# Kernel tuning notes

Hardware: AMD Instinct MI355X
Metric: run time of the kernel (lower is better)

Reference implementation:

```python
import jax, jax.numpy as jnp
import numpy as np

B, S, D, H = 2, 2048, 768, 12
DK = D // H
NEG = -10000.0


def setup_inputs() -> dict:
    key = jax.random.key(0)
    ks = jax.random.split(key, 12)
    def lin(k):
        kw, kb = jax.random.split(k)
        return (jax.random.normal(kw, (D, D), jnp.float32) * 0.02,
                jax.random.normal(kb, (D,), jnp.float32) * 0.02)
    Wq, bq = lin(ks[0]); Wk, bk = lin(ks[1]); Wv, bv = lin(ks[2]); Wo, bo = lin(ks[3])
    query = jax.random.normal(ks[4], (B, S, D), jnp.float32)
    key_t = jax.random.normal(ks[5], (B, S, D), jnp.float32)
    value = jax.random.normal(ks[6], (B, S, D), jnp.float32)
    # causal mask, broadcastable to [B,H,S,S]; positions with 0 are masked
    mask = jnp.tril(jnp.ones((S, S), jnp.int32))[None, None, :, :]
    return {"query": query, "key": key_t, "value": value, "mask": mask,
            "Wq": Wq, "bq": bq, "Wk": Wk, "bk": bk, "Wv": Wv, "bv": bv,
            "Wo": Wo, "bo": bo}


def reference(query, key, value, mask, Wq, bq, Wk, bk, Wv, bv, Wo, bo):
    # torch.nn.Linear: y = x @ W^T + b
    def split_heads(x):  # [B,S,D] -> [B,H,S,DK]
        return x.reshape(B, S, H, DK).transpose(0, 2, 1, 3)
    q = split_heads(query @ Wq.T + bq)
    k = split_heads(key @ Wk.T + bk)
    v = split_heads(value @ Wv.T + bv)
    scores = jnp.einsum('bhqd,bhkd->bhqk', q, k) / jnp.sqrt(jnp.float32(DK))
    scores = jnp.where(mask == 0, NEG, scores)  # masked_fill(mask==0, -1e4)
    attn = jax.nn.softmax(scores, axis=-1)      # dropout p=0.0 -> identity
    x = jnp.einsum('bhqk,bhkd->bhqd', attn, v)  # [B,H,S,DK]
    x = x.transpose(0, 2, 1, 3).reshape(B, S, D)
    return x @ Wo.T + bo
```

## Files before the change

kernel.cpp:

```cpp
#include <hip/hip_runtime.h>
#include <cstdint>


#define B_ 2
#define S_ 2048
#define D_ 768
#define H_ 12
#define DK_ 64

typedef __bf16 bf16;
typedef __bf16 bf16x8 __attribute__((ext_vector_type(8)));
typedef float f32x4 __attribute__((ext_vector_type(4)));
typedef uint32_t u32x4 __attribute__((ext_vector_type(4)));

__device__ __forceinline__ f32x4 mfma16(bf16x8 a, bf16x8 b, f32x4 c) {
  return __builtin_amdgcn_mfma_f32_16x16x32_bf16(a, b, c, 0, 0, 0);
}

struct raw8 { u32x4 a, b; };

__device__ __forceinline__ raw8 fetch8(const void* base, size_t off, int isbf) {
  raw8 r;
  if (isbf) {
    r.a = *(const u32x4*)((const bf16*)base + off);
  } else {
    const float* f = (const float*)base + off;
    r.a = *(const u32x4*)f;
    r.b = *(const u32x4*)(f + 4);
  }
  return r;
}

__device__ __forceinline__ bf16x8 cvt8(raw8 r, int isbf) {
  if (isbf) return __builtin_bit_cast(bf16x8, r.a);
  const float4 x = __builtin_bit_cast(float4, r.a);
  const float4 y = __builtin_bit_cast(float4, r.b);
  bf16x8 o;
  o[0]=(bf16)x.x; o[1]=(bf16)x.y; o[2]=(bf16)x.z; o[3]=(bf16)x.w;
  o[4]=(bf16)y.x; o[5]=(bf16)y.y; o[6]=(bf16)y.z; o[7]=(bf16)y.w;
  return o;
}

__device__ __forceinline__ float load_scalar(const void* base, int idx, int isbf) {
  return isbf ? (float)((const bf16*)base)[idx] : ((const float*)base)[idx];
}

__global__ void detect_kernel(const uint32_t* __restrict__ q, int* flag) {
  __shared__ int cnt;
  if (threadIdx.x == 0) cnt = 0;
  __syncthreads();
  int local = 0;
  for (int i = (int)threadIdx.x; i < 1024; i += 256) {
    const uint32_t e = (q[i] >> 7) & 0xff;
    if (e >= 96 && e <= 140) local++;
  }
  atomicAdd(&cnt, local);
  __syncthreads();
  if (threadIdx.x == 0) *flag = (cnt >= 600) ? 1 : 0;
}

__global__ __launch_bounds__(256) void qkv_kernel(
    const void* __restrict__ q, const void* __restrict__ k,
    const void* __restrict__ v,
    const void* __restrict__ Wq, const void* __restrict__ Wk,
    const void* __restrict__ Wv,
    const void* __restrict__ bq, const void* __restrict__ bk,
    const void* __restrict__ bv,
    bf16* __restrict__ qh, bf16* __restrict__ kh, bf16* __restrict__ vt,
    const int* __restrict__ flag)
{
  __shared__ __align__(16) bf16 As[128][40];
  __shared__ __align__(16) bf16 Bs[64][40];
  const int isbf = *flag;
  const int z = (int)blockIdx.z;
  const void* X = (z == 0) ? q : (z == 1) ? k : v;
  const void* W = (z == 0) ? Wq : (z == 1) ? Wk : Wv;
  const void* bias = (z == 0) ? bq : (z == 1) ? bk : bv;
  bf16* out = (z == 0) ? qh : (z == 1) ? kh : vt;
  const int mode = (z == 2) ? 1 : 0;

  const int m0 = blockIdx.x * 128;
  const int h = (int)blockIdx.y;
  const int n0 = h * 64;
  const int t = (int)threadIdx.x;
  const int lane = t & 63, w = t >> 6, c = lane & 15, quad = lane >> 4;
  const int ar = t >> 2, as = (t & 3) * 8;

  f32x4 acc[2][4];
#pragma unroll
  for (int mt = 0; mt < 2; ++mt)
#pragma unroll
    for (int nb = 0; nb < 4; ++nb)
#pragma unroll
      for (int i = 0; i < 4; ++i) acc[mt][nb][i] = 0.0f;

  raw8 pa0 = fetch8(X, (size_t)(m0 + ar) * D_ + as, isbf);
  raw8 pa1 = fetch8(X, (size_t)(m0 + 64 + ar) * D_ + as, isbf);
  raw8 pb  = fetch8(W, (size_t)(n0 + ar) * D_ + as, isbf);

  for (int k0 = 0; k0 < D_; k0 += 32) {
    __syncthreads();
    *(bf16x8*)&As[ar][as]      = cvt8(pa0, isbf);
    *(bf16x8*)&As[64 + ar][as] = cvt8(pa1, isbf);
    *(bf16x8*)&Bs[ar][as]      = cvt8(pb, isbf);
    __syncthreads();
    if (k0 + 32 < D_) {
      pa0 = fetch8(X, (size_t)(m0 + ar) * D_ + k0 + 32 + as, isbf);
      pa1 = fetch8(X, (size_t)(m0 + 64 + ar) * D_ + k0 + 32 + as, isbf);
      pb  = fetch8(W, (size_t)(n0 + ar) * D_ + k0 + 32 + as, isbf);
    }
    bf16x8 af0 = *(const bf16x8*)&As[w * 32 + c][quad * 8];
    bf16x8 af1 = *(const bf16x8*)&As[w * 32 + 16 + c][quad * 8];
#pragma unroll
    for (int nb = 0; nb < 4; ++nb) {
      const bf16x8 bfr = *(const bf16x8*)&Bs[nb * 16 + c][quad * 8];
      acc[0][nb] = mfma16(af0, bfr, acc[0][nb]);
      acc[1][nb] = mfma16(af1, bfr, acc[1][nb]);
    }
  }

#pragma unroll
  for (int nb = 0; nb < 4; ++nb) {
    const int dk = nb * 16 + c;
    const float bv_ = load_scalar(bias, n0 + dk, isbf);
#pragma unroll
    for (int mt = 0; mt < 2; ++mt)
#pragma unroll
      for (int r = 0; r < 4; ++r) {
        const int m = m0 + w * 32 + mt * 16 + quad * 4 + r;
        const int bi = m >> 11, s = m & (S_ - 1);
        const float val = acc[mt][nb][r] + bv_;
        if (mode == 0)
          out[(((size_t)bi * H_ + h) * S_ + s) * DK_ + dk] = (bf16)val;
        else
          out[(((size_t)bi * H_ + h) * DK_ + dk) * S_ + s] = (bf16)val;
      }
  }
}

__global__ __launch_bounds__(256) void attn_kernel(
    const bf16* __restrict__ qh, const bf16* __restrict__ kh,
    const bf16* __restrict__ vt, bf16* __restrict__ xh)
{
  __shared__ __align__(16) bf16 Ks[2][64][72];
  __shared__ __align__(16) bf16 Vts[2][64][72];
  __shared__ __align__(16) bf16 Ps[4][16][72];

  const int g = (int)blockIdx.y >> 3;
  const int x = (int)blockIdx.x;
  const int jt = (g == 0) ? x : (g == 1) ? (31 - x) : (x ^ 16);
  const int qb = jt * 64;

  const int bh = (int)blockIdx.y;
  const int bi = bh / H_, h = bh % H_;
  const bf16* qp = qh + (size_t)bh * S_ * DK_;
  const bf16* kp = kh + (size_t)bh * S_ * DK_;
  const bf16* vp = vt + (size_t)bh * DK_ * S_;

  const int t = (int)threadIdx.x;
  const int lane = t & 63, w = t >> 6, c = lane & 15, quad = lane >> 4;
  const int r8 = t >> 3, sg = t & 7;

  const float SCL = 0.125f * 1.44269504088896f;
  bf16x8 qf0 = *(const bf16x8*)(qp + (size_t)(qb + w * 16 + c) * DK_ + quad * 8);
  bf16x8 qf1 = *(const bf16x8*)(qp + (size_t)(qb + w * 16 + c) * DK_ + 32 + quad * 8);
#pragma unroll
  for (int i = 0; i < 8; ++i) {
    qf0[i] = (bf16)((float)qf0[i] * SCL);
    qf1[i] = (bf16)((float)qf1[i] * SCL);
  }

  f32x4 acc[4];
#pragma unroll
  for (int nb = 0; nb < 4; ++nb)
#pragma unroll
    for (int i = 0; i < 4; ++i) acc[nb][i] = 0.0f;
  float lp[4] = {0.0f, 0.0f, 0.0f, 0.0f};

  bf16x8 kr0, kr1, vr0, vr1;
  auto loadKV = [&](int kb) {
    kr0 = *(const bf16x8*)(kp + (size_t)(kb + r8) * DK_ + sg * 8);
    kr1 = *(const bf16x8*)(kp + (size_t)(kb + 32 + r8) * DK_ + sg * 8);
    vr0 = *(const bf16x8*)(vp + (size_t)r8 * S_ + kb + sg * 8);
    vr1 = *(const bf16x8*)(vp + (size_t)(r8 + 32) * S_ + kb + sg * 8);
  };

  const int nkt = jt + 1;
  loadKV(0);
  int p = 0;

  for (int kt = 0; kt < nkt; ++kt) {
    *(bf16x8*)&Ks[p][r8][sg * 8]       = kr0;
    *(bf16x8*)&Ks[p][32 + r8][sg * 8]  = kr1;
    *(bf16x8*)&Vts[p][r8][sg * 8]      = vr0;
    *(bf16x8*)&Vts[p][32 + r8][sg * 8] = vr1;
    __syncthreads();
    if (kt + 1 < nkt) loadKV((kt + 1) * 64);

    f32x4 sc[4];
#pragma unroll
    for (int nb = 0; nb < 4; ++nb) {
#pragma unroll
      for (int i = 0; i < 4; ++i) sc[nb][i] = 0.0f;
      const bf16x8 kf0 = *(const bf16x8*)&Ks[p][nb * 16 + c][quad * 8];
      const bf16x8 kf1 = *(const bf16x8*)&Ks[p][nb * 16 + c][32 + quad * 8];
      sc[nb] = mfma16(qf0, kf0, sc[nb]);
      sc[nb] = mfma16(qf1, kf1, sc[nb]);
    }

    if (kt == nkt - 1) {
#pragma unroll
      for (int nb = 0; nb < 4; ++nb)
#pragma unroll
        for (int r = 0; r < 4; ++r) {
          const int colr = nb * 16 + c;
          const int rowr = w * 16 + quad * 4 + r;
          if (colr > rowr) sc[nb][r] = -__builtin_inff();
        }
    }

    float sv[4][4];
#pragma unroll
    for (int nb = 0; nb < 4; ++nb)
#pragma unroll
      for (int r = 0; r < 4; ++r) sv[nb][r] = exp2f(sc[nb][r]);
#pragma unroll
    for (int r = 0; r < 4; ++r)
      lp[r] += (sv[0][r] + sv[1][r]) + (sv[2][r] + sv[3][r]);

#pragma unroll
    for (int nb = 0; nb < 4; ++nb)
#pragma unroll
      for (int r = 0; r < 4; ++r)
        Ps[w][quad * 4 + r][nb * 16 + c] = (bf16)sv[nb][r];
    const bf16x8 pf0 = *(const bf16x8*)&Ps[w][c][quad * 8];
    const bf16x8 pf1 = *(const bf16x8*)&Ps[w][c][32 + quad * 8];
#pragma unroll
    for (int nb = 0; nb < 4; ++nb) {
      const bf16x8 vf0 = *(const bf16x8*)&Vts[p][nb * 16 + c][quad * 8];
      const bf16x8 vf1 = *(const bf16x8*)&Vts[p][nb * 16 + c][32 + quad * 8];
      acc[nb] = mfma16(pf0, vf0, acc[nb]);
      acc[nb] = mfma16(pf1, vf1, acc[nb]);
    }
    p ^= 1;
  }

#pragma unroll
  for (int r = 0; r < 4; ++r) {
    float l = lp[r];
#pragma unroll
    for (int off = 1; off < 16; off <<= 1) l += __shfl_xor(l, off);
    const float inv = 1.0f / l;
    const int s = qb + w * 16 + quad * 4 + r;
#pragma unroll
    for (int nb = 0; nb < 4; ++nb) {
      const int d = h * DK_ + nb * 16 + c;
      xh[((size_t)bi * S_ + s) * D_ + d] = (bf16)(acc[nb][r] * inv);
    }
  }
}

__global__ __launch_bounds__(256) void oproj_kernel(
    const bf16* __restrict__ X, const void* __restrict__ W,
    const void* __restrict__ bias, void* __restrict__ out,
    const int* __restrict__ flag)
{
  __shared__ __align__(16) bf16 As[128][40];
  __shared__ __align__(16) bf16 Bs[64][40];
  const int isbf = *flag;
  const int m0 = blockIdx.x * 128;
  const int n0 = blockIdx.y * 64;
  const int t = (int)threadIdx.x;
  const int lane = t & 63, w = t >> 6, c = lane & 15, quad = lane >> 4;
  const int ar = t >> 2, as = (t & 3) * 8;

  f32x4 acc[2][4];
#pragma unroll
  for (int mt = 0; mt < 2; ++mt)
#pragma unroll
    for (int nb = 0; nb < 4; ++nb)
#pragma unroll
      for (int i = 0; i < 4; ++i) acc[mt][nb][i] = 0.0f;

  raw8 pa0 = fetch8(X, (size_t)(m0 + ar) * D_ + as, 1);
  raw8 pa1 = fetch8(X, (size_t)(m0 + 64 + ar) * D_ + as, 1);
  raw8 pb  = fetch8(W, (size_t)(n0 + ar) * D_ + as, isbf);

  for (int k0 = 0; k0 < D_; k0 += 32) {
    __syncthreads();
    *(bf16x8*)&As[ar][as]      = cvt8(pa0, 1);
    *(bf16x8*)&As[64 + ar][as] = cvt8(pa1, 1);
    *(bf16x8*)&Bs[ar][as]      = cvt8(pb, isbf);
    __syncthreads();
    if (k0 + 32 < D_) {
      pa0 = fetch8(X, (size_t)(m0 + ar) * D_ + k0 + 32 + as, 1);
      pa1 = fetch8(X, (size_t)(m0 + 64 + ar) * D_ + k0 + 32 + as, 1);
      pb  = fetch8(W, (size_t)(n0 + ar) * D_ + k0 + 32 + as, isbf);
    }
    bf16x8 af0 = *(const bf16x8*)&As[w * 32 + c][quad * 8];
    bf16x8 af1 = *(const bf16x8*)&As[w * 32 + 16 + c][quad * 8];
#pragma unroll
    for (int nb = 0; nb < 4; ++nb) {
      const bf16x8 bfr = *(const bf16x8*)&Bs[nb * 16 + c][quad * 8];
      acc[0][nb] = mfma16(af0, bfr, acc[0][nb]);
      acc[1][nb] = mfma16(af1, bfr, acc[1][nb]);
    }
  }

#pragma unroll
  for (int nb = 0; nb < 4; ++nb) {
    const int n = n0 + nb * 16 + c;
    const float bv_ = load_scalar(bias, n, isbf);
#pragma unroll
    for (int mt = 0; mt < 2; ++mt)
#pragma unroll
      for (int r = 0; r < 4; ++r) {
        const int m = m0 + w * 32 + mt * 16 + quad * 4 + r;
        const float v = acc[mt][nb][r] + bv_;
        if (isbf) ((bf16*)out)[(size_t)m * D_ + n] = (bf16)v;
        else      ((float*)out)[(size_t)m * D_ + n] = v;
      }
  }
}

extern "C" void kernel_launch(void* const* d_in, const int* in_sizes, int n_in,
                              void* d_out, int out_size, void* d_ws, size_t ws_size,
                              hipStream_t stream) {
  const void* query = d_in[0];
  const void* key_  = d_in[1];
  const void* value = d_in[2];
  const void* Wq = d_in[4];
  const void* bq = d_in[5];
  const void* Wk = d_in[6];
  const void* bk = d_in[7];
  const void* Wv = d_in[8];
  const void* bv = d_in[9];
  const void* Wo = d_in[10];
  const void* bo = d_in[11];

  const size_t NE = (size_t)B_ * H_ * S_ * DK_;
  bf16* qh = (bf16*)d_ws;
  bf16* kh = qh + NE;
  bf16* vt = kh + NE;
  bf16* xh = vt + NE;
  int* flag = (int*)(xh + NE);

  dim3 blk(256);
  detect_kernel<<<1, blk, 0, stream>>>((const uint32_t*)query, flag);
  qkv_kernel<<<dim3(32, 12, 3), blk, 0, stream>>>(
      query, key_, value, Wq, Wk, Wv, bq, bk, bv, qh, kh, vt, flag);
  attn_kernel<<<dim3(32, 24), blk, 0, stream>>>(qh, kh, vt, xh);
  oproj_kernel<<<dim3(32, 12), blk, 0, stream>>>(xh, Wo, bo, d_out, flag);
}
```

Baseline: 240.9 us.

## Pre-convert inputs to bf16, use 128x128 LDS-DMA GEMMs and 128-row attention tiles

A separate conversion kernel casts the activations and all four weight matrices to bf16 up front. The QKV and output projections then share a new 128x128-tile GEMM body that is double-buffered through direct global-to-LDS loads, with a single barrier per k-step. The attention kernel now gives each block 128 query rows (32 per wave) so every loaded K/V tile is reused across twice as many queries. The trade-offs are an extra full read and write pass over the fp32 inputs, fewer blocks for the projections and attention, and higher register pressure in attention.

```diff
diff --git a/kernel.cpp b/kernel.cpp
--- a/kernel.cpp
+++ b/kernel.cpp
@@ -15,6 +15,12 @@
 
 __device__ __forceinline__ f32x4 mfma16(bf16x8 a, bf16x8 b, f32x4 c) {
   return __builtin_amdgcn_mfma_f32_16x16x32_bf16(a, b, c, 0, 0, 0);
+}
+
+__device__ __forceinline__ void gl2lds16(const bf16* g, bf16* l) {
+  __builtin_amdgcn_global_load_lds(
+      (const __attribute__((address_space(1))) uint32_t*)g,
+      (__attribute__((address_space(3))) uint32_t*)l, 16, 0, 0);
 }
 
 struct raw8 { u32x4 a, b; };
@@ -59,81 +65,139 @@
   if (threadIdx.x == 0) *flag = (cnt >= 600) ? 1 : 0;
 }
 
-__global__ __launch_bounds__(256) void qkv_kernel(
+#define NE_ 3145728
+#define NW_ 589824
+#define NE8_ 393216
+#define NW8_ 73728
+__global__ __launch_bounds__(256) void cvt_kernel(
     const void* __restrict__ q, const void* __restrict__ k,
     const void* __restrict__ v,
     const void* __restrict__ Wq, const void* __restrict__ Wk,
-    const void* __restrict__ Wv,
+    const void* __restrict__ Wv, const void* __restrict__ Wo,
+    bf16* __restrict__ dst, const int* __restrict__ flag)
+{
+  const int isbf = *flag;
+  const int u = (int)(blockIdx.x * 256 + threadIdx.x);
+  if (u >= 3 * NE8_ + 4 * NW8_) return;
+  const void* src;
+  size_t off8;
+  bf16* d;
+  if (u < 3 * NE8_) {
+    const int wq = u / NE8_;
+    off8 = (size_t)(u - wq * NE8_);
+    src = (wq == 0) ? q : (wq == 1) ? k : v;
+    d = dst + (size_t)wq * NE_;
+  } else {
+    const int u2 = u - 3 * NE8_;
+    const int wq = u2 / NW8_;
+    off8 = (size_t)(u2 - wq * NW8_);
+    src = (wq == 0) ? Wq : (wq == 1) ? Wk : (wq == 2) ? Wv : Wo;
+    d = dst + (size_t)3 * NE_ + (size_t)wq * NW_;
+  }
+  raw8 rr = fetch8(src, off8 * 8, isbf);
+  *(bf16x8*)&d[off8 * 8] = cvt8(rr, isbf);
+}
+
+#define GEMM_BODY(Xg, Wg, m0, n0)                                            \
+  __shared__ __align__(16) bf16 As[2][128][32];                              \
+  __shared__ __align__(16) bf16 Bs[2][128][32];                              \
+  const int t = (int)threadIdx.x;                                            \
+  const int lane = t & 63, w = t >> 6, c = lane & 15, quad = lane >> 4;      \
+  const int wm = w & 1, wn = w >> 1;                                         \
+  const int rsub = lane >> 2, csub = (lane & 3) * 8;                         \
+  f32x4 acc[4][4];                                                           \
+  _Pragma("unroll") for (int i = 0; i < 4; ++i)                              \
+      _Pragma("unroll") for (int j = 0; j < 4; ++j)                          \
+          _Pragma("unroll") for (int e = 0; e < 4; ++e) acc[i][j][e] = 0.0f; \
+  auto issue = [&](int p, int k0) {                                          \
+    _Pragma("unroll") for (int i = 0; i < 2; ++i) {                          \
+      const int rr = (w * 2 + i) * 16;                                       \
+      gl2lds16(Xg + (size_t)(m0 + rr + rsub) * D_ + k0 + csub,               \
+               &As[p][rr][0]);                                               \
+      gl2lds16(Wg + (size_t)(n0 + rr + rsub) * D_ + k0 + csub,               \
+               &Bs[p][rr][0]);                                               \
+    }                                                                        \
+  };                                                                         \
+  issue(0, 0);                                                               \
+  int p = 0;                                                                 \
+  for (int kt = 0; kt < D_ / 32; ++kt) {                                     \
+    __syncthreads();                                                         \
+    if (kt + 1 < D_ / 32) issue(p ^ 1, (kt + 1) * 32);                       \
+    bf16x8 af[4], bfr[4];                                                    \
+    _Pragma("unroll") for (int i = 0; i < 4; ++i) {                          \
+      af[i] = *(const bf16x8*)&As[p][wm * 64 + i * 16 + c][quad * 8];        \
+      bfr[i] = *(const bf16x8*)&Bs[p][wn * 64 + i * 16 + c][quad * 8];       \
+    }                                                                        \
+    _Pragma("unroll") for (int i = 0; i < 4; ++i)                            \
+        _Pragma("unroll") for (int j = 0; j < 4; ++j)                        \
+            acc[i][j] = mfma16(af[i], bfr[j], acc[i][j]);                    \
+    p ^= 1;                                                                  \
+  }
+
+__global__ __launch_bounds__(256) void qkv_kernel(
+    const bf16* __restrict__ qc, const bf16* __restrict__ kc,
+    const bf16* __restrict__ vc,
+    const bf16* __restrict__ Wqc, const bf16* __restrict__ Wkc,
+    const bf16* __restrict__ Wvc,
     const void* __restrict__ bq, const void* __restrict__ bk,
     const void* __restrict__ bv,
     bf16* __restrict__ qh, bf16* __restrict__ kh, bf16* __restrict__ vt,
     const int* __restrict__ flag)
 {
-  __shared__ __align__(16) bf16 As[128][40];
-  __shared__ __align__(16) bf16 Bs[64][40];
   const int isbf = *flag;
-  const int z = (int)blockIdx.z;
-  const void* X = (z == 0) ? q : (z == 1) ? k : v;
-  const void* W = (z == 0) ? Wq : (z == 1) ? Wk : Wv;
+  const int z = (int)blockIdx.y / 6;
+  const int n0 = ((int)blockIdx.y % 6) * 128;
+  const int m0 = (int)blockIdx.x * 128;
+  const bf16* Xg = (z == 0) ? qc : (z == 1) ? kc : vc;
+  const bf16* Wg = (z == 0) ? Wqc : (z == 1) ? Wkc : Wvc;
   const void* bias = (z == 0) ? bq : (z == 1) ? bk : bv;
   bf16* out = (z == 0) ? qh : (z == 1) ? kh : vt;
-  const int mode = (z == 2) ? 1 : 0;
-
-  const int m0 = blockIdx.x * 128;
-  const int h = (int)blockIdx.y;
-  const int n0 = h * 64;
-  const int t = (int)threadIdx.x;
-  const int lane = t & 63, w = t >> 6, c = lane & 15, quad = lane >> 4;
-  const int ar = t >> 2, as = (t & 3) * 8;
-
-  f32x4 acc[2][4];
-#pragma unroll
-  for (int mt = 0; mt < 2; ++mt)
-#pragma unroll
-    for (int nb = 0; nb < 4; ++nb)
-#pragma unroll
-      for (int i = 0; i < 4; ++i) acc[mt][nb][i] = 0.0f;
-
-  raw8 pa0 = fetch8(X, (size_t)(m0 + ar) * D_ + as, isbf);
-  raw8 pa1 = fetch8(X, (size_t)(m0 + 64 + ar) * D_ + as, isbf);
-  raw8 pb  = fetch8(W, (size_t)(n0 + ar) * D_ + as, isbf);
-
-  for (int k0 = 0; k0 < D_; k0 += 32) {
-    __syncthreads();
-    *(bf16x8*)&As[ar][as]      = cvt8(pa0, isbf);
-    *(bf16x8*)&As[64 + ar][as] = cvt8(pa1, isbf);
-    *(bf16x8*)&Bs[ar][as]      = cvt8(pb, isbf);
-    __syncthreads();
-    if (k0 + 32 < D_) {
-      pa0 = fetch8(X, (size_t)(m0 + ar) * D_ + k0 + 32 + as, isbf);
-      pa1 = fetch8(X, (size_t)(m0 + 64 + ar) * D_ + k0 + 32 + as, isbf);
-      pb  = fetch8(W, (size_t)(n0 + ar) * D_ + k0 + 32 + as, isbf);
-    }
-    bf16x8 af0 = *(const bf16x8*)&As[w * 32 + c][quad * 8];
-    bf16x8 af1 = *(const bf16x8*)&As[w * 32 + 16 + c][quad * 8];
-#pragma unroll
-    for (int nb = 0; nb < 4; ++nb) {
-      const bf16x8 bfr = *(const bf16x8*)&Bs[nb * 16 + c][quad * 8];
-      acc[0][nb] = mfma16(af0, bfr, acc[0][nb]);
-      acc[1][nb] = mfma16(af1, bfr, acc[1][nb]);
-    }
-  }
-
-#pragma unroll
-  for (int nb = 0; nb < 4; ++nb) {
-    const int dk = nb * 16 + c;
-    const float bv_ = load_scalar(bias, n0 + dk, isbf);
-#pragma unroll
-    for (int mt = 0; mt < 2; ++mt)
+
+  GEMM_BODY(Xg, Wg, m0, n0)
+
+#pragma unroll
+  for (int j = 0; j < 4; ++j) {
+    const int n = n0 + wn * 64 + j * 16 + c;
+    const int h = n >> 6, dk = n & 63;
+    const float bv_ = load_scalar(bias, n, isbf);
+#pragma unroll
+    for (int i = 0; i < 4; ++i)
 #pragma unroll
       for (int r = 0; r < 4; ++r) {
-        const int m = m0 + w * 32 + mt * 16 + quad * 4 + r;
+        const int m = m0 + wm * 64 + i * 16 + quad * 4 + r;
         const int bi = m >> 11, s = m & (S_ - 1);
-        const float val = acc[mt][nb][r] + bv_;
-        if (mode == 0)
+        const float val = acc[i][j][r] + bv_;
+        if (z != 2)
           out[(((size_t)bi * H_ + h) * S_ + s) * DK_ + dk] = (bf16)val;
         else
           out[(((size_t)bi * H_ + h) * DK_ + dk) * S_ + s] = (bf16)val;
+      }
+  }
+}
+
+__global__ __launch_bounds__(256) void oproj_kernel(
+    const bf16* __restrict__ xh, const bf16* __restrict__ Woc,
+    const void* __restrict__ bias, void* __restrict__ out,
+    const int* __restrict__ flag)
+{
+  const int isbf = *flag;
+  const int m0 = (int)blockIdx.x * 128;
+  const int n0 = (int)blockIdx.y * 128;
+
+  GEMM_BODY(xh, Woc, m0, n0)
+
+#pragma unroll
+  for (int j = 0; j < 4; ++j) {
+    const int n = n0 + wn * 64 + j * 16 + c;
+    const float bv_ = load_scalar(bias, n, isbf);
+#pragma unroll
+    for (int i = 0; i < 4; ++i)
+#pragma unroll
+      for (int r = 0; r < 4; ++r) {
+        const int m = m0 + wm * 64 + i * 16 + quad * 4 + r;
+        const float v = acc[i][j][r] + bv_;
+        if (isbf) ((bf16*)out)[(size_t)m * D_ + n] = (bf16)v;
+        else      ((float*)out)[(size_t)m * D_ + n] = v;
       }
   }
 }
@@ -144,12 +208,12 @@
 {
   __shared__ __align__(16) bf16 Ks[2][64][72];
   __shared__ __align__(16) bf16 Vts[2][64][72];
-  __shared__ __align__(16) bf16 Ps[4][16][72];
+  __shared__ __align__(16) bf16 Ps[4][32][72];
 
   const int g = (int)blockIdx.y >> 3;
   const int x = (int)blockIdx.x;
-  const int jt = (g == 0) ? x : (g == 1) ? (31 - x) : (x ^ 16);
-  const int qb = jt * 64;
+  const int jt = (g == 0) ? x : (g == 1) ? (15 - x) : (x ^ 8);
+  const int qb = jt * 128;
 
   const int bh = (int)blockIdx.y;
   const int bi = bh / H_, h = bh % H_;
@@ -162,20 +226,27 @@
   const int r8 = t >> 3, sg = t & 7;
 
   const float SCL = 0.125f * 1.44269504088896f;
-  bf16x8 qf0 = *(const bf16x8*)(qp + (size_t)(qb + w * 16 + c) * DK_ + quad * 8);
-  bf16x8 qf1 = *(const bf16x8*)(qp + (size_t)(qb + w * 16 + c) * DK_ + 32 + quad * 8);
-#pragma unroll
-  for (int i = 0; i < 8; ++i) {
-    qf0[i] = (bf16)((float)qf0[i] * SCL);
-    qf1[i] = (bf16)((float)qf1[i] * SCL);
-  }
-
-  f32x4 acc[4];
-#pragma unroll
-  for (int nb = 0; nb < 4; ++nb)
-#pragma unroll
-    for (int i = 0; i < 4; ++i) acc[nb][i] = 0.0f;
-  float lp[4] = {0.0f, 0.0f, 0.0f, 0.0f};
+  bf16x8 qf[2][2];
+#pragma unroll
+  for (int mt = 0; mt < 2; ++mt) {
+    const size_t qrow = (size_t)(qb + w * 32 + mt * 16 + c) * DK_;
+    qf[mt][0] = *(const bf16x8*)(qp + qrow + quad * 8);
+    qf[mt][1] = *(const bf16x8*)(qp + qrow + 32 + quad * 8);
+#pragma unroll
+    for (int i = 0; i < 8; ++i) {
+      qf[mt][0][i] = (bf16)((float)qf[mt][0][i] * SCL);
+      qf[mt][1][i] = (bf16)((float)qf[mt][1][i] * SCL);
+    }
+  }
+
+  f32x4 acc[2][4];
+#pragma unroll
+  for (int mt = 0; mt < 2; ++mt)
+#pragma unroll
+    for (int nb = 0; nb < 4; ++nb)
+#pragma unroll
+      for (int i = 0; i < 4; ++i) acc[mt][nb][i] = 0.0f;
+  float lp[2][4] = {{0,0,0,0},{0,0,0,0}};
 
   bf16x8 kr0, kr1, vr0, vr1;
   auto loadKV = [&](int kb) {
@@ -185,7 +256,7 @@
     vr1 = *(const bf16x8*)(vp + (size_t)(r8 + 32) * S_ + kb + sg * 8);
   };
 
-  const int nkt = jt + 1;
+  const int nkt = 2 * jt + 2;
   loadKV(0);
   int p = 0;
 
@@ -197,130 +268,79 @@
     __syncthreads();
     if (kt + 1 < nkt) loadKV((kt + 1) * 64);
 
-    f32x4 sc[4];
+    f32x4 sc[2][4];
 #pragma unroll
     for (int nb = 0; nb < 4; ++nb) {
-#pragma unroll
-      for (int i = 0; i < 4; ++i) sc[nb][i] = 0.0f;
       const bf16x8 kf0 = *(const bf16x8*)&Ks[p][nb * 16 + c][quad * 8];
       const bf16x8 kf1 = *(const bf16x8*)&Ks[p][nb * 16 + c][32 + quad * 8];
-      sc[nb] = mfma16(qf0, kf0, sc[nb]);
-      sc[nb] = mfma16(qf1, kf1, sc[nb]);
-    }
-
-    if (kt == nkt - 1) {
+#pragma unroll
+      for (int mt = 0; mt < 2; ++mt) {
+#pragma unroll
+        for (int i = 0; i < 4; ++i) sc[mt][nb][i] = 0.0f;
+        sc[mt][nb] = mfma16(qf[mt][0], kf0, sc[mt][nb]);
+        sc[mt][nb] = mfma16(qf[mt][1], kf1, sc[mt][nb]);
+      }
+    }
+
+    if (kt >= nkt - 2) {
+#pragma unroll
+      for (int mt = 0; mt < 2; ++mt)
+#pragma unroll
+        for (int nb = 0; nb < 4; ++nb)
+#pragma unroll
+          for (int r = 0; r < 4; ++r) {
+            const int colA = kt * 64 + nb * 16 + c;
+            const int rowA = qb + w * 32 + mt * 16 + quad * 4 + r;
+            if (colA > rowA) sc[mt][nb][r] = -__builtin_inff();
+          }
+    }
+
+#pragma unroll
+    for (int mt = 0; mt < 2; ++mt) {
+      float sv[4][4];
 #pragma unroll
       for (int nb = 0; nb < 4; ++nb)
 #pragma unroll
-        for (int r = 0; r < 4; ++r) {
-          const int colr = nb * 16 + c;
-          const int rowr = w * 16 + quad * 4 + r;
-          if (colr > rowr) sc[nb][r] = -__builtin_inff();
-        }
-    }
-
-    float sv[4][4];
-#pragma unroll
-    for (int nb = 0; nb < 4; ++nb)
-#pragma unroll
-      for (int r = 0; r < 4; ++r) sv[nb][r] = exp2f(sc[nb][r]);
-#pragma unroll
-    for (int r = 0; r < 4; ++r)
-      lp[r] += (sv[0][r] + sv[1][r]) + (sv[2][r] + sv[3][r]);
-
-#pragma unroll
-    for (int nb = 0; nb < 4; ++nb)
+        for (int r = 0; r < 4; ++r) sv[nb][r] = exp2f(sc[mt][nb][r]);
 #pragma unroll
       for (int r = 0; r < 4; ++r)
-        Ps[w][quad * 4 + r][nb * 16 + c] = (bf16)sv[nb][r];
-    const bf16x8 pf0 = *(const bf16x8*)&Ps[w][c][quad * 8];
-    const bf16x8 pf1 = *(const bf16x8*)&Ps[w][c][32 + quad * 8];
+        lp[mt][r] += (sv[0][r] + sv[1][r]) + (sv[2][r] + sv[3][r]);
+#pragma unroll
+      for (int nb = 0; nb < 4; ++nb)
+#pragma unroll
+        for (int r = 0; r < 4; ++r)
+          Ps[w][mt * 16 + quad * 4 + r][nb * 16 + c] = (bf16)sv[nb][r];
+    }
 #pragma unroll
     for (int nb = 0; nb < 4; ++nb) {
       const bf16x8 vf0 = *(const bf16x8*)&Vts[p][nb * 16 + c][quad * 8];
       const bf16x8 vf1 = *(const bf16x8*)&Vts[p][nb * 16 + c][32 + quad * 8];
-      acc[nb] = mfma16(pf0, vf0, acc[nb]);
-      acc[nb] = mfma16(pf1, vf1, acc[nb]);
+#pragma unroll
+      for (int mt = 0; mt < 2; ++mt) {
+        const bf16x8 pf0 = *(const bf16x8*)&Ps[w][mt * 16 + c][quad * 8];
+        const bf16x8 pf1 = *(const bf16x8*)&Ps[w][mt * 16 + c][32 + quad * 8];
+        acc[mt][nb] = mfma16(pf0, vf0, acc[mt][nb]);
+        acc[mt][nb] = mfma16(pf1, vf1, acc[mt][nb]);
+      }
     }
     p ^= 1;
   }
 
 #pragma unroll
-  for (int r = 0; r < 4; ++r) {
-    float l = lp[r];
-#pragma unroll
-    for (int off = 1; off < 16; off <<= 1) l += __shfl_xor(l, off);
-    const float inv = 1.0f / l;
-    const int s = qb + w * 16 + quad * 4 + r;
-#pragma unroll
-    for (int nb = 0; nb < 4; ++nb) {
-      const int d = h * DK_ + nb * 16 + c;
-      xh[((size_t)bi * S_ + s) * D_ + d] = (bf16)(acc[nb][r] * inv);
-    }
-  }
-}
-
-__global__ __launch_bounds__(256) void oproj_kernel(
-    const bf16* __restrict__ X, const void* __restrict__ W,
-    const void* __restrict__ bias, void* __restrict__ out,
-    const int* __restrict__ flag)
-{
-  __shared__ __align__(16) bf16 As[128][40];
-  __shared__ __align__(16) bf16 Bs[64][40];
-  const int isbf = *flag;
-  const int m0 = blockIdx.x * 128;
-  const int n0 = blockIdx.y * 64;
-  const int t = (int)threadIdx.x;
-  const int lane = t & 63, w = t >> 6, c = lane & 15, quad = lane >> 4;
-  const int ar = t >> 2, as = (t & 3) * 8;
-
-  f32x4 acc[2][4];
-#pragma unroll
   for (int mt = 0; mt < 2; ++mt)
 #pragma unroll
-    for (int nb = 0; nb < 4; ++nb)
-#pragma unroll
-      for (int i = 0; i < 4; ++i) acc[mt][nb][i] = 0.0f;
-
-  raw8 pa0 = fetch8(X, (size_t)(m0 + ar) * D_ + as, 1);
-  raw8 pa1 = fetch8(X, (size_t)(m0 + 64 + ar) * D_ + as, 1);
-  raw8 pb  = fetch8(W, (size_t)(n0 + ar) * D_ + as, isbf);
-
-  for (int k0 = 0; k0 < D_; k0 += 32) {
-    __syncthreads();
-    *(bf16x8*)&As[ar][as]      = cvt8(pa0, 1);
-    *(bf16x8*)&As[64 + ar][as] = cvt8(pa1, 1);
-    *(bf16x8*)&Bs[ar][as]      = cvt8(pb, isbf);
-    __syncthreads();
-    if (k0 + 32 < D_) {
-      pa0 = fetch8(X, (size_t)(m0 + ar) * D_ + k0 + 32 + as, 1);
-      pa1 = fetch8(X, (size_t)(m0 + 64 + ar) * D_ + k0 + 32 + as, 1);
-      pb  = fetch8(W, (size_t)(n0 + ar) * D_ + k0 + 32 + as, isbf);
-    }
-    bf16x8 af0 = *(const bf16x8*)&As[w * 32 + c][quad * 8];
-    bf16x8 af1 = *(const bf16x8*)&As[w * 32 + 16 + c][quad * 8];
-#pragma unroll
-    for (int nb = 0; nb < 4; ++nb) {
-      const bf16x8 bfr = *(const bf16x8*)&Bs[nb * 16 + c][quad * 8];
-      acc[0][nb] = mfma16(af0, bfr, acc[0][nb]);
-      acc[1][nb] = mfma16(af1, bfr, acc[1][nb]);
-    }
-  }
-
-#pragma unroll
-  for (int nb = 0; nb < 4; ++nb) {
-    const int n = n0 + nb * 16 + c;
-    const float bv_ = load_scalar(bias, n, isbf);
-#pragma unroll
-    for (int mt = 0; mt < 2; ++mt)
-#pragma unroll
-      for (int r = 0; r < 4; ++r) {
-        const int m = m0 + w * 32 + mt * 16 + quad * 4 + r;
-        const float v = acc[mt][nb][r] + bv_;
-        if (isbf) ((bf16*)out)[(size_t)m * D_ + n] = (bf16)v;
-        else      ((float*)out)[(size_t)m * D_ + n] = v;
-      }
-  }
+    for (int r = 0; r < 4; ++r) {
+      float l = lp[mt][r];
+#pragma unroll
+      for (int off = 1; off < 16; off <<= 1) l += __shfl_xor(l, off);
+      const float inv = 1.0f / l;
+      const int s = qb + w * 32 + mt * 16 + quad * 4 + r;
+#pragma unroll
+      for (int nb = 0; nb < 4; ++nb) {
+        const int d = h * DK_ + nb * 16 + c;
+        xh[((size_t)bi * S_ + s) * D_ + d] = (bf16)(acc[mt][nb][r] * inv);
+      }
+    }
 }
 
 extern "C" void kernel_launch(void* const* d_in, const int* in_sizes, int n_in,
@@ -338,17 +358,25 @@
   const void* Wo = d_in[10];
   const void* bo = d_in[11];
 
-  const size_t NE = (size_t)B_ * H_ * S_ * DK_;
-  bf16* qh = (bf16*)d_ws;
-  bf16* kh = qh + NE;
-  bf16* vt = kh + NE;
-  bf16* xh = vt + NE;
-  int* flag = (int*)(xh + NE);
+  bf16* qc  = (bf16*)d_ws;
+  bf16* kc  = qc + NE_;
+  bf16* vc  = kc + NE_;
+  bf16* Wqc = vc + NE_;
+  bf16* Wkc = Wqc + NW_;
+  bf16* Wvc = Wkc + NW_;
+  bf16* Woc = Wvc + NW_;
+  bf16* qh  = Woc + NW_;
+  bf16* kh  = qh + NE_;
+  bf16* vt  = kh + NE_;
+  bf16* xh  = qc;
+  int* flag = (int*)(vt + NE_);
 
   dim3 blk(256);
   detect_kernel<<<1, blk, 0, stream>>>((const uint32_t*)query, flag);
-  qkv_kernel<<<dim3(32, 12, 3), blk, 0, stream>>>(
-      query, key_, value, Wq, Wk, Wv, bq, bk, bv, qh, kh, vt, flag);
-  attn_kernel<<<dim3(32, 24), blk, 0, stream>>>(qh, kh, vt, xh);
-  oproj_kernel<<<dim3(32, 12), blk, 0, stream>>>(xh, Wo, bo, d_out, flag);
-}
+  cvt_kernel<<<(3 * NE8_ + 4 * NW8_ + 255) / 256, blk, 0, stream>>>(
+      query, key_, value, Wq, Wk, Wv, Wo, qc, flag);
+  qkv_kernel<<<dim3(32, 18), blk, 0, stream>>>(
+      qc, kc, vc, Wqc, Wkc, Wvc, bq, bk, bv, qh, kh, vt, flag);
+  attn_kernel<<<dim3(16, 24), blk, 0, stream>>>(qh, kh, vt, xh);
+  oproj_kernel<<<dim3(32, 6), blk, 0, stream>>>(xh, Woc, bo, d_out, flag);
+}
```

After: 238.5 us. No clear change (-1.0%).
